# Performance work log

Hardware: AMD Instinct MI355X
Metric: run time of the kernel (lower is better)

Reference implementation:

```python
import jax, jax.numpy as jnp
import numpy as np
import math

B = 32        # graphs in batch
N_PER = 2000  # nodes per graph
E_PER = 16000 # edges per graph
H = 256       # hidden_size
EF = 20       # edge_features
ET = 3        # edge_types
C = 100       # candidate nodes per graph
N = B * N_PER
E = B * E_PER


def setup_inputs() -> dict:
    key = jax.random.key(0)
    ks = jax.random.split(key, 12)
    embedding = jax.random.normal(ks[0], (N, H), dtype=jnp.float32)
    scores = jax.random.normal(ks[1], (N, 1), dtype=jnp.float32)
    offsets = jnp.arange(B, dtype=jnp.int64) * N_PER
    src = (jax.random.randint(ks[2], (B, E_PER), 0, N_PER) + offsets[:, None]).reshape(-1)
    dst = (jax.random.randint(ks[3], (B, E_PER), 0, N_PER) + offsets[:, None]).reshape(-1)
    etype = jax.random.randint(ks[4], (E,), 0, ET)
    cand_idx = offsets[:, None] + jnp.arange(C, dtype=jnp.int64)[None, :]  # [B, C]
    label = jax.random.randint(ks[5], (B,), 0, C)
    s = 1.0 / math.sqrt(H)
    Wl = jax.random.normal(ks[6], (H, H), dtype=jnp.float32) * s
    bl = jnp.zeros((H,), dtype=jnp.float32)
    Wr = jax.random.normal(ks[7], (H, H), dtype=jnp.float32) * s
    br = jnp.zeros((H,), dtype=jnp.float32)
    We = jax.random.normal(ks[8], (H, EF), dtype=jnp.float32) * (1.0 / math.sqrt(EF))
    be = jnp.zeros((H,), dtype=jnp.float32)
    edge_emb = jax.random.normal(ks[9], (ET, EF), dtype=jnp.float32)
    return {"embedding": embedding, "scores": scores, "Wl": Wl, "bl": bl,
            "Wr": Wr, "br": br, "We": We, "be": be, "edge_emb": edge_emb,
            "src": src, "dst": dst, "etype": etype, "cand_idx": cand_idx,
            "label": label}


def reference(embedding, scores, Wl, bl, Wr, br, We, be, edge_emb,
              src, dst, etype, cand_idx, label):
    # dropout is identity in eval mode
    h = embedding
    # edge type features: GELU(Embedding(type))  (torch GELU = exact erf form)
    ef = jax.nn.gelu(edge_emb[etype], approximate=False)          # [E, EF]
    attn_q = h @ Wl.T + bl                                         # [N, H]
    attn_k1 = h @ Wr.T + br                                        # [N, H]
    attn_k2 = ef @ We.T + be                                       # [E, H]
    # u_add_e: src node key + edge key
    attn_k = attn_k1[src] + attn_k2                                # [E, H]
    # v_dot_e: dst query dot edge key, scaled
    alpha = jnp.sum(attn_q[dst] * attn_k, axis=-1) / jnp.sqrt(jnp.float32(H))  # [E]
    # edge_softmax over incoming edges of each dst node
    seg_max = jax.ops.segment_max(alpha, dst, num_segments=N)
    ex = jnp.exp(alpha - seg_max[dst])
    seg_sum = jax.ops.segment_sum(ex, dst, num_segments=N)
    a = ex / seg_sum[dst]                                          # [E]
    # u_mul_e + sum aggregation: scatter-sum of src scores weighted by attention
    upd = jax.ops.segment_sum(scores[src] * a[:, None], dst, num_segments=N)  # [N, 1]
    # per-graph candidate logits and CE loss
    logits = upd[cand_idx.reshape(-1)].reshape(B, C)               # [B, C]
    logp = jax.nn.log_softmax(logits, axis=-1)
    loss = -jnp.sum(logp[jnp.arange(B), label])
    return loss, logits
```

## Files before the change

### kernel.cpp

```cpp
#include <hip/hip_runtime.h>
#include <hip/hip_bf16.h>
#include <float.h>
#include <math.h>

#define NB 32
#define NPER 2000
#define EPER 16000
#define HID 256
#define EFD 20
#define ETN 3
#define CN 100
#define NTOT (NB*NPER)
#define ETOT (NB*EPER)

#define QDELTA (6.0f/127.0f)
#define QINV   (127.0f/6.0f)

using f32x4  = __attribute__((ext_vector_type(4))) float;
using bf16x8 = __attribute__((ext_vector_type(8))) short;
using ushort8= __attribute__((ext_vector_type(8))) unsigned short;
using u32x4  = __attribute__((ext_vector_type(4))) unsigned int;

__device__ __forceinline__ unsigned short f2bf(float f){
  union{float f; unsigned int i;}v; v.f=f; unsigned int x=v.i;
  return (unsigned short)((x + 0x7fffu + ((x>>16)&1u)) >> 16);
}
__device__ __forceinline__ unsigned int cvt_pk_bf16(float lo, float hi){
  unsigned int r;
  asm("v_cvt_pk_bf16_f32 %0, %1, %2" : "=v"(r) : "v"(lo), "v"(hi));
  return r;
}
__device__ __forceinline__ void dot4i8(int& acc, unsigned int a, unsigned int b){
  asm("v_dot4_i32_i8 %0, %1, %2, %0" : "+v"(acc) : "v"(a), "v"(b));
}

__global__ __launch_bounds__(256) void setup_kernel(
    const float* __restrict__ Wl, const float* __restrict__ Wr,
    const float* __restrict__ We, const float* __restrict__ be,
    const float* __restrict__ edge_emb,
    unsigned short* __restrict__ Wlsw, unsigned short* __restrict__ Wrsw,
    signed char* __restrict__ k2q, float* __restrict__ k2scale,
    float* __restrict__ segsum, float* __restrict__ wsum, float* __restrict__ out)
{
  __shared__ float k2f[ETN*HID];
  __shared__ float redmax[256];
  int b = blockIdx.x, t = threadIdx.x;
  if (b < 250) {
    int i = b*256 + t;
    segsum[i] = 0.0f; wsum[i] = 0.0f;
    if (i == 0) out[0] = 0.0f;
  } else if (b < 314) {
    int u = (b-250)*256 + t;
    int mat  = u >> 13;
    int v    = u & 8191;
    int cblk = v >> 9;
    int r    = v & 511;
    int kblk = r >> 6;
    int lane = r & 63;
    int col  = (cblk<<4) | (lane&15);
    int kk   = (kblk<<5) | ((lane>>4)<<3);
    const float* Wsrc = mat ? Wr : Wl;
    const f32x4* p = (const f32x4*)(Wsrc + col*HID + kk);
    f32x4 x0 = p[0], x1 = p[1];
    ushort8 w;
    w[0]=f2bf(x0[0]); w[1]=f2bf(x0[1]); w[2]=f2bf(x0[2]); w[3]=f2bf(x0[3]);
    w[4]=f2bf(x1[0]); w[5]=f2bf(x1[1]); w[6]=f2bf(x1[2]); w[7]=f2bf(x1[3]);
    *(ushort8*)((mat ? Wrsw : Wlsw) + (size_t)v*8) = w;
  } else {
    int j = t;
    float lmax = 0.0f;
    for (int ty=0; ty<ETN; ty++){
      float acc = be[j];
      for (int f=0; f<EFD; f++){
        float x = edge_emb[ty*EFD+f];
        float g = 0.5f*x*(1.0f + erff(x*0.7071067811865476f));
        acc += g * We[j*EFD+f];
      }
      k2f[ty*HID + j] = acc;
      lmax = fmaxf(lmax, fabsf(acc));
    }
    redmax[t] = lmax; __syncthreads();
    for (int sd=128; sd>0; sd>>=1){
      if (t < sd) redmax[t] = fmaxf(redmax[t], redmax[t+sd]);
      __syncthreads();
    }
    float d2 = fmaxf(redmax[0], 1e-20f) * (1.0f/127.0f);
    for (int ty=0; ty<ETN; ty++){
      int qv = (int)rintf(k2f[ty*HID+j] / d2);
      qv = min(127, max(-127, qv));
      k2q[ty*HID + j] = (signed char)qv;
    }
    if (t == 0) k2scale[0] = d2;
  }
}

#define BM 64
#define BK 64
#define LDA 72

__global__ __launch_bounds__(512) void gemm_qk(
    const float* __restrict__ h,
    const unsigned short* __restrict__ Wlsw, const unsigned short* __restrict__ Wrsw,
    const float* __restrict__ bl, const float* __restrict__ br,
    signed char* __restrict__ Qi8, signed char* __restrict__ K1i8)
{
  __shared__ unsigned short As[BM*LDA];

  int bm = blockIdx.x;
  int tid = threadIdx.x;
  int lane = tid & 63;
  int wv = tid >> 6;
  int wm = wv >> 2;
  int wn = wv & 3;

  f32x4 accQ[2][4], accK[2][4];
  #pragma unroll
  for(int i=0;i<2;i++)
    #pragma unroll
    for(int j=0;j<4;j++)
      #pragma unroll
      for(int r=0;r<4;r++){ accQ[i][j][r]=0.0f; accK[i][j][r]=0.0f; }

  const float* Arow = h + (size_t)bm*BM*HID;
  int arow = tid >> 3;
  int acs  = (tid & 7) * 8;

  #pragma unroll
  for (int kt = 0; kt < 4; ++kt) {
    int k0 = kt*BK;
    f32x4 a0 = *(const f32x4*)(Arow + arow*HID + k0 + acs);
    f32x4 a1 = *(const f32x4*)(Arow + arow*HID + k0 + acs + 4);
    u32x4 aw;
    aw[0] = cvt_pk_bf16(a0[0], a0[1]);
    aw[1] = cvt_pk_bf16(a0[2], a0[3]);
    aw[2] = cvt_pk_bf16(a1[0], a1[1]);
    aw[3] = cvt_pk_bf16(a1[2], a1[3]);
    *(u32x4*)(&As[arow*LDA + acs]) = aw;
    __syncthreads();

    #pragma unroll
    for (int ks = 0; ks < 2; ++ks) {
      int kblk = kt*2 + ks;
      int kb = ks*32 + (lane>>4)*8;
      bf16x8 af[2], lf[4], rf[4];
      #pragma unroll
      for (int fm=0; fm<2; fm++){
        int r0 = wm*32 + fm*16 + (lane&15);
        af[fm] = *(const bf16x8*)(&As[r0*LDA + kb]);
      }
      #pragma unroll
      for (int fn=0; fn<4; fn++){
        int cblk = wn*4 + fn;
        size_t o = ((size_t)(cblk*8 + kblk)*64 + lane)*8;
        lf[fn] = *(const bf16x8*)(Wlsw + o);
        rf[fn] = *(const bf16x8*)(Wrsw + o);
      }
      #pragma unroll
      for (int fm=0; fm<2; fm++)
        #pragma unroll
        for (int fn=0; fn<4; fn++){
          accQ[fm][fn] = __builtin_amdgcn_mfma_f32_16x16x32_bf16(af[fm], lf[fn], accQ[fm][fn], 0,0,0);
          accK[fm][fn] = __builtin_amdgcn_mfma_f32_16x16x32_bf16(af[fm], rf[fn], accK[fm][fn], 0,0,0);
        }
    }
    __syncthreads();
  }

  #pragma unroll
  for (int fn=0; fn<4; fn++){
    int col = wn*64 + fn*16 + (lane&15);
    float blv = bl[col], brv = br[col];
    #pragma unroll
    for (int fm=0; fm<2; fm++){
      int row0 = bm*BM + wm*32 + fm*16 + ((lane>>4)<<2);
      #pragma unroll
      for (int r=0; r<4; r++){
        size_t o = (size_t)(row0+r)*HID + col;
        int qv = (int)rintf((accQ[fm][fn][r] + blv) * QINV);
        int kv = (int)rintf((accK[fm][fn][r] + brv) * QINV);
        Qi8[o]  = (signed char)min(127, max(-127, qv));
        K1i8[o] = (signed char)min(127, max(-127, kv));
      }
    }
  }
}

__global__ __launch_bounds__(256) void tdot_kernel(
    const signed char* __restrict__ Qi8, const signed char* __restrict__ k2q,
    const float* __restrict__ k2scale, float* __restrict__ T)
{
  __shared__ unsigned int k2s[ETN*64];
  for (int i=threadIdx.x; i<ETN*64; i+=256)
    k2s[i] = ((const unsigned int*)k2q)[i];
  __syncthreads();

  int tid = threadIdx.x;
  int sl = tid & 15;
  int n = blockIdx.x*16 + (tid>>4);
  u32x4 q  = ((const u32x4*)(Qi8 + (size_t)n*HID))[sl];
  u32x4 c0 = ((const u32x4*)(k2s))[sl];
  u32x4 c1 = ((const u32x4*)(k2s + 64))[sl];
  u32x4 c2 = ((const u32x4*)(k2s + 128))[sl];
  int a0=0, a1=0, a2=0;
  #pragma unroll
  for (int w2=0; w2<4; w2++){
    dot4i8(a0, q[w2], c0[w2]);
    dot4i8(a1, q[w2], c1[w2]);
    dot4i8(a2, q[w2], c2[w2]);
  }
  #pragma unroll
  for (int m=1;m<16;m<<=1){
    a0 += __shfl_xor(a0, m);
    a1 += __shfl_xor(a1, m);
    a2 += __shfl_xor(a2, m);
  }
  if (sl==0){
    float sc = QDELTA * k2scale[0];
    f32x4 tv; tv[0]=a0*sc; tv[1]=a1*sc; tv[2]=a2*sc; tv[3]=0.f;
    *(f32x4*)(T + (size_t)n*4) = tv;
  }
}

__global__ __launch_bounds__(256) void edge_attn(
    const signed char* __restrict__ Qi8, const signed char* __restrict__ K1i8,
    const float* __restrict__ T,
    const int* __restrict__ src, const int* __restrict__ dst, const int* __restrict__ ety,
    const float* __restrict__ scores,
    float* __restrict__ segsum, float* __restrict__ wsum)
{
  int bid = blockIdx.x;
  int xcd = bid & 7;
  int slot = bid >> 3;
  int grp = slot / 500;
  int within = slot - grp*500;
  int graph = grp*8 + xcd;

  int tid = threadIdx.x;
  int sl = tid & 15;
  int g = tid >> 4;
  int ebase = graph*EPER + within*32;
  int e0 = ebase + g;
  int e1 = ebase + 16 + g;

  int s0 = src[e0], d0 = dst[e0], t0 = ety[e0];
  int s1 = src[e1], d1 = dst[e1], t1 = ety[e1];

  u32x4 q0 = ((const u32x4*)(Qi8  + (size_t)d0*HID))[sl];
  u32x4 k0 = ((const u32x4*)(K1i8 + (size_t)s0*HID))[sl];
  u32x4 q1 = ((const u32x4*)(Qi8  + (size_t)d1*HID))[sl];
  u32x4 k1 = ((const u32x4*)(K1i8 + (size_t)s1*HID))[sl];

  int acc0=0, acc1=0;
  #pragma unroll
  for (int w2=0; w2<4; w2++){
    dot4i8(acc0, q0[w2], k0[w2]);
    dot4i8(acc1, q1[w2], k1[w2]);
  }
  #pragma unroll
  for (int m=1;m<16;m<<=1){
    acc0 += __shfl_xor(acc0, m);
    acc1 += __shfl_xor(acc1, m);
  }
  if (sl==0){
    const float DD = QDELTA*QDELTA;
    float ex0 = expf((acc0*DD + T[(size_t)d0*4 + t0]) * 0.0625f);
    float ex1 = expf((acc1*DD + T[(size_t)d1*4 + t1]) * 0.0625f);
    atomicAdd(&segsum[d0], ex0);
    atomicAdd(&wsum[d0], ex0 * scores[s0]);
    atomicAdd(&segsum[d1], ex1);
    atomicAdd(&wsum[d1], ex1 * scores[s1]);
  }
}

__global__ __launch_bounds__(128) void logits_kernel(
    const float* __restrict__ segsum, const float* __restrict__ wsum,
    const int* __restrict__ cand, const int* __restrict__ label,
    float* __restrict__ out)
{
  __shared__ float red[128];
  __shared__ float lvals[CN];
  int b = blockIdx.x;
  int t = threadIdx.x;
  float v = -FLT_MAX;
  if (t < CN){
    int node = cand[b*CN + t];
    float ss = segsum[node];
    float u = (ss > 0.0f) ? (wsum[node]/ss) : 0.0f;
    lvals[t] = u;
    out[1 + b*CN + t] = u;
    v = u;
  }
  red[t] = v; __syncthreads();
  for (int sd=64; sd>0; sd>>=1){
    if (t < sd) red[t] = fmaxf(red[t], red[t+sd]);
    __syncthreads();
  }
  float mx = red[0];
  __syncthreads();
  float sv = (t < CN) ? expf(lvals[t]-mx) : 0.0f;
  red[t] = sv; __syncthreads();
  for (int sd=64; sd>0; sd>>=1){
    if (t < sd) red[t] += red[t+sd];
    __syncthreads();
  }
  if (t==0){
    float lse = mx + logf(red[0]);
    atomicAdd(out, -(lvals[label[b]] - lse));
  }
}

extern "C" void kernel_launch(void* const* d_in, const int* in_sizes, int n_in,
                              void* d_out, int out_size, void* d_ws, size_t ws_size,
                              hipStream_t stream) {
  const float* emb      = (const float*)d_in[0];
  const float* scores   = (const float*)d_in[1];
  const float* Wl       = (const float*)d_in[2];
  const float* blb      = (const float*)d_in[3];
  const float* Wr       = (const float*)d_in[4];
  const float* brb      = (const float*)d_in[5];
  const float* We       = (const float*)d_in[6];
  const float* be       = (const float*)d_in[7];
  const float* edge_emb = (const float*)d_in[8];
  const int* src   = (const int*)d_in[9];
  const int* dst   = (const int*)d_in[10];
  const int* ety   = (const int*)d_in[11];
  const int* cand  = (const int*)d_in[12];
  const int* label = (const int*)d_in[13];
  float* out = (float*)d_out;

  char* w = (char*)d_ws;
  size_t off = 0;
  auto alloc = [&](size_t bytes)->char* {
    char* p = w + off; off += (bytes + 255) & ~(size_t)255; return p;
  };
  signed char*    Qi8  = (signed char*)alloc((size_t)NTOT*HID);
  signed char*    K1i8 = (signed char*)alloc((size_t)NTOT*HID);
  unsigned short* Wlsw = (unsigned short*)alloc((size_t)HID*HID*2);
  unsigned short* Wrsw = (unsigned short*)alloc((size_t)HID*HID*2);
  signed char*    k2q  = (signed char*)alloc((size_t)ETN*HID);
  float* k2scale = (float*)alloc(4);
  float* T      = (float*)alloc((size_t)NTOT*4*4);
  float* segsum = (float*)alloc((size_t)NTOT*4);
  float* wsum   = (float*)alloc((size_t)NTOT*4);
  (void)ws_size; (void)in_sizes; (void)n_in; (void)out_size;

  setup_kernel<<<dim3(315), dim3(256), 0, stream>>>(Wl, Wr, We, be, edge_emb,
                                                    Wlsw, Wrsw, k2q, k2scale, segsum, wsum, out);
  gemm_qk<<<dim3(NTOT/BM), dim3(512), 0, stream>>>(emb, Wlsw, Wrsw, blb, brb, Qi8, K1i8);
  tdot_kernel<<<dim3(NTOT/16), dim3(256), 0, stream>>>(Qi8, k2q, k2scale, T);
  edge_attn<<<dim3(ETOT/32), dim3(256), 0, stream>>>(Qi8, K1i8, T, src, dst, ety, scores,
                                                     segsum, wsum);
  logits_kernel<<<dim3(NB), dim3(128), 0, stream>>>(segsum, wsum, cand, label, out);
}
```

Before: 222.5 us.

## Interleave segment accumulators, process four edges per lane group, prefetch GEMM A tiles

The two per-node accumulators (softmax denominator and weighted score sum) are merged into one interleaved array, so both atomics for a destination node hit the same cache line. The edge kernel now handles four edges per 16-lane group, loading indices as int4 vectors, and spreads the atomics across eight lanes instead of serializing four atomics on one lane. The GEMM prefetches the next A tile into registers before the MFMA loop, so global loads overlap with compute. The cost is more live registers in both kernels, which may lower occupancy, and half as many blocks in the edge kernel.

Measured after the change: 199.2 us. 10.5% less time.

```diff
diff --git a/kernel.cpp b/kernel.cpp
--- a/kernel.cpp
+++ b/kernel.cpp
@@ -33,6 +33,13 @@
 __device__ __forceinline__ void dot4i8(int& acc, unsigned int a, unsigned int b){
   asm("v_dot4_i32_i8 %0, %1, %2, %0" : "+v"(acc) : "v"(a), "v"(b));
 }
+__device__ __forceinline__ int sel4(int4 v, int i){
+  int r = v.x;
+  r = (i==1) ? v.y : r;
+  r = (i==2) ? v.z : r;
+  r = (i==3) ? v.w : r;
+  return r;
+}
 
 __global__ __launch_bounds__(256) void setup_kernel(
     const float* __restrict__ Wl, const float* __restrict__ Wr,
@@ -40,17 +47,17 @@
     const float* __restrict__ edge_emb,
     unsigned short* __restrict__ Wlsw, unsigned short* __restrict__ Wrsw,
     signed char* __restrict__ k2q, float* __restrict__ k2scale,
-    float* __restrict__ segsum, float* __restrict__ wsum, float* __restrict__ out)
+    float* __restrict__ seg, float* __restrict__ out)
 {
   __shared__ float k2f[ETN*HID];
   __shared__ float redmax[256];
   int b = blockIdx.x, t = threadIdx.x;
-  if (b < 250) {
+  if (b < 500) {
     int i = b*256 + t;
-    segsum[i] = 0.0f; wsum[i] = 0.0f;
+    seg[i] = 0.0f;
     if (i == 0) out[0] = 0.0f;
-  } else if (b < 314) {
-    int u = (b-250)*256 + t;
+  } else if (b < 564) {
+    int u = (b-500)*256 + t;
     int mat  = u >> 13;
     int v    = u & 8191;
     int cblk = v >> 9;
@@ -125,18 +132,23 @@
   int arow = tid >> 3;
   int acs  = (tid & 7) * 8;
 
+  f32x4 cur0 = *(const f32x4*)(Arow + arow*HID + acs);
+  f32x4 cur1 = *(const f32x4*)(Arow + arow*HID + acs + 4);
+
   #pragma unroll
   for (int kt = 0; kt < 4; ++kt) {
-    int k0 = kt*BK;
-    f32x4 a0 = *(const f32x4*)(Arow + arow*HID + k0 + acs);
-    f32x4 a1 = *(const f32x4*)(Arow + arow*HID + k0 + acs + 4);
     u32x4 aw;
-    aw[0] = cvt_pk_bf16(a0[0], a0[1]);
-    aw[1] = cvt_pk_bf16(a0[2], a0[3]);
-    aw[2] = cvt_pk_bf16(a1[0], a1[1]);
-    aw[3] = cvt_pk_bf16(a1[2], a1[3]);
+    aw[0] = cvt_pk_bf16(cur0[0], cur0[1]);
+    aw[1] = cvt_pk_bf16(cur0[2], cur0[3]);
+    aw[2] = cvt_pk_bf16(cur1[0], cur1[1]);
+    aw[3] = cvt_pk_bf16(cur1[2], cur1[3]);
     *(u32x4*)(&As[arow*LDA + acs]) = aw;
     __syncthreads();
+
+    if (kt < 3) {
+      cur0 = *(const f32x4*)(Arow + arow*HID + (kt+1)*BK + acs);
+      cur1 = *(const f32x4*)(Arow + arow*HID + (kt+1)*BK + acs + 4);
+    }
 
     #pragma unroll
     for (int ks = 0; ks < 2; ++ks) {
@@ -226,54 +238,67 @@
     const float* __restrict__ T,
     const int* __restrict__ src, const int* __restrict__ dst, const int* __restrict__ ety,
     const float* __restrict__ scores,
-    float* __restrict__ segsum, float* __restrict__ wsum)
+    float* __restrict__ seg)
 {
   int bid = blockIdx.x;
   int xcd = bid & 7;
   int slot = bid >> 3;
-  int grp = slot / 500;
-  int within = slot - grp*500;
+  int grp = slot / 250;
+  int within = slot - grp*250;
   int graph = grp*8 + xcd;
 
   int tid = threadIdx.x;
   int sl = tid & 15;
   int g = tid >> 4;
-  int ebase = graph*EPER + within*32;
-  int e0 = ebase + g;
-  int e1 = ebase + 16 + g;
-
-  int s0 = src[e0], d0 = dst[e0], t0 = ety[e0];
-  int s1 = src[e1], d1 = dst[e1], t1 = ety[e1];
-
-  u32x4 q0 = ((const u32x4*)(Qi8  + (size_t)d0*HID))[sl];
-  u32x4 k0 = ((const u32x4*)(K1i8 + (size_t)s0*HID))[sl];
-  u32x4 q1 = ((const u32x4*)(Qi8  + (size_t)d1*HID))[sl];
-  u32x4 k1 = ((const u32x4*)(K1i8 + (size_t)s1*HID))[sl];
-
-  int acc0=0, acc1=0;
+  int e0 = graph*EPER + within*64 + g*4;
+
+  int4 sv4 = *(const int4*)(src + e0);
+  int4 dv4 = *(const int4*)(dst + e0);
+  int4 tv4 = *(const int4*)(ety + e0);
+
+  u32x4 q0 = ((const u32x4*)(Qi8  + (size_t)dv4.x*HID))[sl];
+  u32x4 k0 = ((const u32x4*)(K1i8 + (size_t)sv4.x*HID))[sl];
+  u32x4 q1 = ((const u32x4*)(Qi8  + (size_t)dv4.y*HID))[sl];
+  u32x4 k1 = ((const u32x4*)(K1i8 + (size_t)sv4.y*HID))[sl];
+  u32x4 q2 = ((const u32x4*)(Qi8  + (size_t)dv4.z*HID))[sl];
+  u32x4 k2 = ((const u32x4*)(K1i8 + (size_t)sv4.z*HID))[sl];
+  u32x4 q3 = ((const u32x4*)(Qi8  + (size_t)dv4.w*HID))[sl];
+  u32x4 k3 = ((const u32x4*)(K1i8 + (size_t)sv4.w*HID))[sl];
+
+  int a0=0, a1=0, a2=0, a3=0;
   #pragma unroll
   for (int w2=0; w2<4; w2++){
-    dot4i8(acc0, q0[w2], k0[w2]);
-    dot4i8(acc1, q1[w2], k1[w2]);
+    dot4i8(a0, q0[w2], k0[w2]);
+    dot4i8(a1, q1[w2], k1[w2]);
+    dot4i8(a2, q2[w2], k2[w2]);
+    dot4i8(a3, q3[w2], k3[w2]);
   }
   #pragma unroll
   for (int m=1;m<16;m<<=1){
-    acc0 += __shfl_xor(acc0, m);
-    acc1 += __shfl_xor(acc1, m);
-  }
-  if (sl==0){
+    a0 += __shfl_xor(a0, m);
+    a1 += __shfl_xor(a1, m);
+    a2 += __shfl_xor(a2, m);
+    a3 += __shfl_xor(a3, m);
+  }
+  if (sl < 8){
+    int j = sl & 3;
+    int role = sl >> 2;
+    int dn = sel4(dv4, j);
+    int sn = sel4(sv4, j);
+    int tn = sel4(tv4, j);
+    float av = (float)a0;
+    av = (j==1) ? (float)a1 : av;
+    av = (j==2) ? (float)a2 : av;
+    av = (j==3) ? (float)a3 : av;
     const float DD = QDELTA*QDELTA;
-    float ex0 = expf((acc0*DD + T[(size_t)d0*4 + t0]) * 0.0625f);
-    float ex1 = expf((acc1*DD + T[(size_t)d1*4 + t1]) * 0.0625f);
-    atomicAdd(&segsum[d0], ex0);
-    atomicAdd(&wsum[d0], ex0 * scores[s0]);
-    atomicAdd(&segsum[d1], ex1);
-    atomicAdd(&wsum[d1], ex1 * scores[s1]);
+    float ex = expf((av*DD + T[(size_t)dn*4 + tn]) * 0.0625f);
+    float val = role ? ex * scores[sn] : ex;
+    atomicAdd(&seg[2*dn + role], val);
   }
 }
 
 __global__ __launch_bounds__(128) void logits_kernel(
-    const float* __restrict__ segsum, const float* __restrict__ wsum,
+    const float* __restrict__ seg,
     const int* __restrict__ cand, const int* __restrict__ label,
     float* __restrict__ out)
 {
@@ -284,8 +309,8 @@
   float v = -FLT_MAX;
   if (t < CN){
     int node = cand[b*CN + t];
-    float ss = segsum[node];
-    float u = (ss > 0.0f) ? (wsum[node]/ss) : 0.0f;
+    float ss = seg[2*node];
+    float u = (ss > 0.0f) ? (seg[2*node+1]/ss) : 0.0f;
     lvals[t] = u;
     out[1 + b*CN + t] = u;
     v = u;
@@ -340,15 +365,14 @@
   signed char*    k2q  = (signed char*)alloc((size_t)ETN*HID);
   float* k2scale = (float*)alloc(4);
   float* T      = (float*)alloc((size_t)NTOT*4*4);
-  float* segsum = (float*)alloc((size_t)NTOT*4);
-  float* wsum   = (float*)alloc((size_t)NTOT*4);
+  float* seg    = (float*)alloc((size_t)NTOT*8);
   (void)ws_size; (void)in_sizes; (void)n_in; (void)out_size;
 
-  setup_kernel<<<dim3(315), dim3(256), 0, stream>>>(Wl, Wr, We, be, edge_emb,
-                                                    Wlsw, Wrsw, k2q, k2scale, segsum, wsum, out);
+  setup_kernel<<<dim3(565), dim3(256), 0, stream>>>(Wl, Wr, We, be, edge_emb,
+                                                    Wlsw, Wrsw, k2q, k2scale, seg, out);
   gemm_qk<<<dim3(NTOT/BM), dim3(512), 0, stream>>>(emb, Wlsw, Wrsw, blb, brb, Qi8, K1i8);
   tdot_kernel<<<dim3(NTOT/16), dim3(256), 0, stream>>>(Qi8, k2q, k2scale, T);
-  edge_attn<<<dim3(ETOT/32), dim3(256), 0, stream>>>(Qi8, K1i8, T, src, dst, ety, scores,
-                                                     segsum, wsum);
-  logits_kernel<<<dim3(NB), dim3(128), 0, stream>>>(segsum, wsum, cand, label, out);
-}
+  edge_attn<<<dim3(ETOT/64), dim3(256), 0, stream>>>(Qi8, K1i8, T, src, dst, ety, scores,
+                                                     seg);
+  logits_kernel<<<dim3(NB), dim3(128), 0, stream>>>(seg, cand, label, out);
+}
```
